# Performance work log

Measured on AMD Instinct MI355X. Metric: run time of the kernel, lower is better.

Reference implementation:

```python
import jax, jax.numpy as jnp
import numpy as np

N = 25000      # nodes
E = 400000     # edges (before self-loops)
D = 64         # input node feature dim
H = 4          # attention heads
C = 64         # out channels per head (concat=False -> head mean)
L = 3          # stacked layers
NEG_SLOPE = 0.2
EPS = 1e-5


def setup_inputs() -> dict:
    key = jax.random.key(0)
    ks = jax.random.split(key, 8)
    s = 0.1
    return {
        "x": jax.random.normal(ks[0], (N, D), jnp.float32),
        "edge_index": jax.random.randint(ks[1], (2, E), 0, N, dtype=jnp.int64),
        "Wl": jax.random.normal(ks[2], (L, H * C, D), jnp.float32) * s,
        "bl": jnp.zeros((L, H * C), jnp.float32),
        "Wr": jax.random.normal(ks[3], (L, H * C, D), jnp.float32) * s,
        "br": jnp.zeros((L, H * C), jnp.float32),
        "att": jax.random.normal(ks[4], (L, H, C), jnp.float32) * s,
        "conv_bias": jnp.zeros((L, C), jnp.float32),
        "gn_weight": jnp.ones((L, C), jnp.float32),
        "gn_scale": jnp.ones((L, C), jnp.float32),   # GraphNorm mean_scale (alpha)
        "gn_bias": jnp.zeros((L, C), jnp.float32),
    }


def _gat_forward(x, src, dst, Wl, bl, Wr, br, att, conv_bias,
                 gn_weight, gn_scale, gn_bias):
    n = x.shape[0]
    for i in range(L):
        # GATv2Conv (edge_attr=None, concat=False): separate source/target projections
        xl = (x @ Wl[i].T + bl[i]).reshape(n, H, C)  # [N,H,C]
        xr = (x @ Wr[i].T + br[i]).reshape(n, H, C)
        # per-edge attention logits: att . leaky_relu(xl[j] + xr[i])
        e = jax.nn.leaky_relu(xl[src] + xr[dst], NEG_SLOPE)      # [E',H,C]
        logits = jnp.einsum('ehc,hc->eh', e, att[i])             # [E',H]
        # segment softmax over incoming edges of each target node
        m = jax.ops.segment_max(logits, dst, num_segments=n)     # [N,H]
        a = jnp.exp(logits - m[dst])
        denom = jax.ops.segment_sum(a, dst, num_segments=n)      # [N,H]
        alpha = a / denom[dst]                                   # [E',H]
        # weighted scatter-add of source messages, mean over heads
        agg = jax.ops.segment_sum(xl[src] * alpha[:, :, None], dst,
                                  num_segments=n)                # [N,H,C]
        h = agg.mean(axis=1) + conv_bias[i]                      # [N,C]
        # GraphNorm (single graph): x - alpha*mean, scale by rstd
        mu = h.mean(axis=0)
        hc = h - gn_scale[i] * mu
        var = jnp.mean(hc * hc, axis=0)
        x = hc * jax.lax.rsqrt(var + EPS) * gn_weight[i] + gn_bias[i]
        # Dropout p=0 at eval -> identity
    return x


def reference(x, edge_index, Wl, bl, Wr, br, att, conv_bias,
              gn_weight, gn_scale, gn_bias):
    n = x.shape[0]
    loop = jnp.arange(n, dtype=edge_index.dtype)
    # PyG GATv2Conv adds self-loops by default
    src = jnp.concatenate([edge_index[0], loop])
    dst = jnp.concatenate([edge_index[1], loop])
    return _gat_forward(x, src, dst, Wl, bl, Wr, br, att, conv_bias,
                        gn_weight, gn_scale, gn_bias)
```

## Files before the change

### kernel.cpp

```cpp
#include <hip/hip_runtime.h>
#include <hip/hip_fp16.h>
#include <math.h>

#define HC   256
#define DD   64
#define CC   64
#define NLAY 3

#define RCAP    64
#define RCAP_SH 6

#define NBKT 64

typedef _Float16 h2 __attribute__((ext_vector_type(2)));
typedef _Float16 h4 __attribute__((ext_vector_type(4)));
typedef _Float16 h8 __attribute__((ext_vector_type(8)));
typedef float    f4 __attribute__((ext_vector_type(4)));
typedef float    f2 __attribute__((ext_vector_type(2)));

#define XSTR 72
#define OSTR 276

__global__ __launch_bounds__(256) void zero_kernel(int* __restrict__ counts,
                                                   float* __restrict__ spart,
                                                   int n) {
    int i = blockIdx.x * 256 + threadIdx.x;
    if (i < n) counts[i] = 0;
    if (i < NLAY * NBKT * 128) spart[i] = 0.f;
}

__global__ __launch_bounds__(256) void fill_kernel(const int* __restrict__ srcArr,
                                                   const int* __restrict__ dstArr,
                                                   int* __restrict__ counts,
                                                   int* __restrict__ csr_src,
                                                   int e, int n) {
    int i = blockIdx.x * 256 + threadIdx.x;
    if (i >= e + n) return;
    int s, d;
    if (i < e) { s = srcArr[i]; d = dstArr[i]; }
    else       { s = d = i - e; }
    int slot = atomicAdd(&counts[d], 1);
    if (slot < RCAP) csr_src[(d << RCAP_SH) + slot] = s;
}

__global__ __launch_bounds__(256) void proj_kernel(const float* __restrict__ x,
                                                   const float* __restrict__ Wl,
                                                   const float* __restrict__ bl,
                                                   const float* __restrict__ Wr,
                                                   const float* __restrict__ br,
                                                   __half* __restrict__ xl,
                                                   __half* __restrict__ xr, int n,
                                                   const float* __restrict__ spart,
                                                   const float* __restrict__ pgw,
                                                   const float* __restrict__ pgs,
                                                   const float* __restrict__ pgb) {
    __shared__ _Float16 xs[64 * XSTR];
    __shared__ _Float16 ws[256 * XSTR];
    __shared__ float nrm_a[64], nrm_b[64];
    __shared__ float sred[128];
    const int t  = threadIdx.x;
    const int n0 = blockIdx.x * 64;

    if (spart && t < 128) {
        float a = 0.f;
        #pragma unroll 8
        for (int r = 0; r < NBKT; ++r) a += spart[r * 128 + t];
        sred[t] = a;
    }
    __syncthreads();
    if (t < 64) {
        float a = 1.f, b = 0.f;
        if (spart) {
            float inv_n = 1.0f / (float)n;
            float mu  = sred[t] * inv_n;
            float eh2 = sred[64 + t] * inv_n;
            float al  = pgs[t];
            float var = eh2 - 2.f * al * mu * mu + al * al * mu * mu;
            float rstd = rsqrtf(var + 1e-5f);
            a = pgw[t] * rstd;
            b = pgb[t] - al * mu * a;
        }
        nrm_a[t] = a; nrm_b[t] = b;
    }
    __syncthreads();

    {
        const float* xb = x + (size_t)n0 * DD;
        const int limit = (n - n0) * DD;
        #pragma unroll
        for (int it = 0; it < 4; ++it) {
            int f = (it * 256 + t) * 4;
            float4 v = make_float4(0.f, 0.f, 0.f, 0.f);
            if (f + 3 < limit) v = *(const float4*)(xb + f);
            else {
                float tmp[4] = {0.f, 0.f, 0.f, 0.f};
                for (int q = 0; q < 4; ++q) if (f + q < limit) tmp[q] = xb[f + q];
                v = make_float4(tmp[0], tmp[1], tmp[2], tmp[3]);
            }
            int d = f & 63;
            const float4 a4 = *(const float4*)&nrm_a[d];
            const float4 b4 = *(const float4*)&nrm_b[d];
            h4 hv;
            hv.x = (_Float16)fmaf(v.x, a4.x, b4.x);
            hv.y = (_Float16)fmaf(v.y, a4.y, b4.y);
            hv.z = (_Float16)fmaf(v.z, a4.z, b4.z);
            hv.w = (_Float16)fmaf(v.w, a4.w, b4.w);
            *(h4*)&xs[(f >> 6) * XSTR + d] = hv;
        }
    }

    const int w = t >> 6, lane = t & 63, m = lane & 15, q = lane >> 4;

    h8 A0, A1;
    f4 acc[16];

    #define STAGE_W(Wsel)                                                     \
    {                                                                         \
        _Pragma("unroll")                                                     \
        for (int it = 0; it < 16; ++it) {                                     \
            int f = (it * 256 + t) * 4;                                       \
            float4 v = *(const float4*)((Wsel) + f);                          \
            h4 hv = { (_Float16)v.x, (_Float16)v.y, (_Float16)v.z,            \
                      (_Float16)v.w };                                        \
            *(h4*)&ws[(f >> 6) * XSTR + (f & 63)] = hv;                       \
        }                                                                     \
    }

    #define MFMA_PASS()                                                       \
    {                                                                         \
        _Pragma("unroll")                                                     \
        for (int ct = 0; ct < 16; ++ct) {                                     \
            const _Float16* brow = ws + (ct * 16 + m) * XSTR + q * 8;         \
            const h8 B0 = *(const h8*)brow;                                   \
            const h8 B1 = *(const h8*)(brow + 32);                            \
            f4 c = {0.f, 0.f, 0.f, 0.f};                                      \
            c = __builtin_amdgcn_mfma_f32_16x16x32_f16(A0, B0, c, 0, 0, 0);   \
            c = __builtin_amdgcn_mfma_f32_16x16x32_f16(A1, B1, c, 0, 0, 0);   \
            acc[ct] = c;                                                      \
        }                                                                     \
    }

    #define EPILOGUE(bsel, osel)                                              \
    {                                                                         \
        _Pragma("unroll")                                                     \
        for (int ct = 0; ct < 16; ++ct) {                                     \
            int ch = ct * 16 + m;                                             \
            float bv = (bsel)[ch];                                            \
            _Pragma("unroll")                                                 \
            for (int r = 0; r < 4; ++r)                                       \
                ws[(w * 16 + q * 4 + r) * OSTR + ch] =                        \
                    (_Float16)(acc[ct][r] + bv);                              \
        }                                                                     \
        __syncthreads();                                                      \
        _Pragma("unroll")                                                     \
        for (int it = 0; it < 8; ++it) {                                      \
            int f   = (it * 256 + t) * 8;                                     \
            int row = f >> 8, ch = f & 255;                                   \
            if (n0 + row < n)                                                 \
                *(uint4*)((osel) + (size_t)(n0 + row) * HC + ch) =            \
                    *(const uint4*)&ws[row * OSTR + ch];                      \
        }                                                                     \
    }

    STAGE_W(Wl)
    __syncthreads();
    {
        const _Float16* arow = xs + (w * 16 + m) * XSTR + q * 8;
        A0 = *(const h8*)arow;
        A1 = *(const h8*)(arow + 32);
    }
    MFMA_PASS()
    __syncthreads();
    EPILOGUE(bl, xl)
    __syncthreads();

    STAGE_W(Wr)
    __syncthreads();
    MFMA_PASS()
    __syncthreads();
    EPILOGUE(br, xr)

    #undef STAGE_W
    #undef MFMA_PASS
    #undef EPILOGUE
}

__global__ __launch_bounds__(256) void attn_kernel(const __half* __restrict__ xl,
                                                   const __half* __restrict__ xr,
                                                   const float* __restrict__ att,
                                                   const float* __restrict__ conv_bias,
                                                   const int* __restrict__ counts,
                                                   const int* __restrict__ csr_src,
                                                   float* __restrict__ h_out,
                                                   float* __restrict__ spart, int n) {
    __shared__ float ps[4][64], ps2[4][64];
    const int wave = threadIdx.x >> 6;
    const int l    = threadIdx.x & 63;
    const int v    = blockIdx.x * 4 + wave;
    const bool active = (v < n);

    const int e2 = l >> 5;
    const int h  = (l >> 3) & 3;
    const int co = l & 7;
    const int choff = h * CC + co * 8;

    if (active) {
        h2 xr2[4];
        *(uint4*)xr2 = *(const uint4*)(xr + (size_t)v * HC + choff);
        h2 at2[4];
        {
            const float* ap = att + choff;
            float4 a0 = *(const float4*)(ap);
            float4 a1 = *(const float4*)(ap + 4);
            at2[0] = (h2){(_Float16)a0.x, (_Float16)a0.y};
            at2[1] = (h2){(_Float16)a0.z, (_Float16)a0.w};
            at2[2] = (h2){(_Float16)a1.x, (_Float16)a1.y};
            at2[3] = (h2){(_Float16)a1.z, (_Float16)a1.w};
        }
        const _Float16 k02 = (_Float16)0.2f;

        const int rs = v << RCAP_SH;
        const int re = rs + counts[v];

        float s = 0.f;
        h2 acch[4];
        #pragma unroll
        for (int q = 0; q < 4; ++q) acch[q] = (h2){(_Float16)0.f, (_Float16)0.f};

        #define CLAMPI(i) (((i) < re) ? (i) : rs)

        uint4 r0 = *(const uint4*)(xl + (size_t)csr_src[CLAMPI(rs + e2)]     * HC + choff);
        uint4 r1 = *(const uint4*)(xl + (size_t)csr_src[CLAMPI(rs + 2 + e2)] * HC + choff);
        uint4 r2 = *(const uint4*)(xl + (size_t)csr_src[CLAMPI(rs + 4 + e2)] * HC + choff);
        int jnA = csr_src[CLAMPI(rs + 6 + e2)];
        int jnB = csr_src[CLAMPI(rs + 8 + e2)];
        int jnC = csr_src[CLAMPI(rs + 10 + e2)];

        #define STAGE(RBUF, JREG, VOFF, JOFF)                                 \
        {                                                                     \
            const uint4 cur = RBUF;                                           \
            RBUF = *(const uint4*)(xl + (size_t)JREG * HC + choff);           \
            JREG = csr_src[CLAMPI(k + JOFF + e2)];                            \
            const bool valid = (k + VOFF + e2) < re;                          \
            const h2* xh = (const h2*)&cur;                                   \
            h2 d2 = (h2){(_Float16)0.f, (_Float16)0.f};                      \
            _Pragma("unroll")                                                 \
            for (int q = 0; q < 4; ++q) {                                     \
                h2 tt = xh[q] + xr2[q];                                       \
                h2 lk = __builtin_elementwise_max(tt, tt * k02);              \
                d2 += lk * at2[q];                                            \
            }                                                                 \
            float p = (float)d2.x + (float)d2.y;                              \
            p += __shfl_xor(p, 1, 64);                                        \
            p += __shfl_xor(p, 2, 64);                                        \
            p += __shfl_xor(p, 4, 64);                                        \
            float pe = valid ? __expf(p) : 0.f;                               \
            s += pe;                                                          \
            const _Float16 peh = (_Float16)pe;                                \
            const h2 pe2 = (h2){peh, peh};                                    \
            _Pragma("unroll")                                                 \
            for (int q = 0; q < 4; ++q)                                       \
                acch[q] += pe2 * xh[q];                                       \
        }

        for (int k = rs; k < re; k += 6) {
            STAGE(r0, jnA, 0, 12)
            STAGE(r1, jnB, 2, 14)
            STAGE(r2, jnC, 4, 16)
        }
        #undef STAGE
        #undef CLAMPI

        s += __shfl_xor(s, 32, 64);
        const float inv = 1.f / s;
        float out8[8];
        #pragma unroll
        for (int q = 0; q < 8; ++q) {
            float av = (q & 1) ? (float)acch[q >> 1].y : (float)acch[q >> 1].x;
            float a = av + __shfl_xor(av, 32, 64);
            a *= inv;
            a += __shfl_xor(a, 8, 64);
            a += __shfl_xor(a, 16, 64);
            out8[q] = 0.25f * a;
        }
        if (l < 8) {
            const float4 cb0 = *(const float4*)(conv_bias + co * 8);
            const float4 cb1 = *(const float4*)(conv_bias + co * 8 + 4);
            float4 o0 = make_float4(out8[0] + cb0.x, out8[1] + cb0.y,
                                    out8[2] + cb0.z, out8[3] + cb0.w);
            float4 o1 = make_float4(out8[4] + cb1.x, out8[5] + cb1.y,
                                    out8[6] + cb1.z, out8[7] + cb1.w);
            float* op = h_out + (size_t)v * CC + co * 8;
            *(float4*)op       = o0;
            *(float4*)(op + 4) = o1;
            ps [wave][co * 8 + 0] = o0.x;  ps2[wave][co * 8 + 0] = o0.x * o0.x;
            ps [wave][co * 8 + 1] = o0.y;  ps2[wave][co * 8 + 1] = o0.y * o0.y;
            ps [wave][co * 8 + 2] = o0.z;  ps2[wave][co * 8 + 2] = o0.z * o0.z;
            ps [wave][co * 8 + 3] = o0.w;  ps2[wave][co * 8 + 3] = o0.w * o0.w;
            ps [wave][co * 8 + 4] = o1.x;  ps2[wave][co * 8 + 4] = o1.x * o1.x;
            ps [wave][co * 8 + 5] = o1.y;  ps2[wave][co * 8 + 5] = o1.y * o1.y;
            ps [wave][co * 8 + 6] = o1.z;  ps2[wave][co * 8 + 6] = o1.z * o1.z;
            ps [wave][co * 8 + 7] = o1.w;  ps2[wave][co * 8 + 7] = o1.w * o1.w;
        }
    } else if (l < 8) {
        #pragma unroll
        for (int q = 0; q < 8; ++q) { ps[wave][l * 8 + q] = 0.f; ps2[wave][l * 8 + q] = 0.f; }
    }
    __syncthreads();
    if (threadIdx.x < 128) {
        const int c = threadIdx.x & 63;
        const float (*src)[64] = (threadIdx.x < 64) ? ps : ps2;
        float sum = src[0][c] + src[1][c] + src[2][c] + src[3][c];
        atomicAdd(&spart[(blockIdx.x & (NBKT - 1)) * 128 +
                         ((threadIdx.x < 64) ? c : 64 + c)], sum);
    }
}

__global__ __launch_bounds__(256) void norm_kernel(const float* __restrict__ h,
                                                   const float* __restrict__ spart,
                                                   const float* __restrict__ gw,
                                                   const float* __restrict__ gs,
                                                   const float* __restrict__ gb,
                                                   float* __restrict__ out, int n) {
    __shared__ float sred[128];
    __shared__ float na[64], nb[64];
    int t = threadIdx.x;
    if (t < 128) {
        float a = 0.f;
        #pragma unroll 8
        for (int r = 0; r < NBKT; ++r) a += spart[r * 128 + t];
        sred[t] = a;
    }
    __syncthreads();
    if (t < 64) {
        float inv_n = 1.0f / (float)n;
        float mu  = sred[t] * inv_n;
        float eh2 = sred[64 + t] * inv_n;
        float a   = gs[t];
        float var = eh2 - 2.f * a * mu * mu + a * a * mu * mu;
        float rstd = rsqrtf(var + 1e-5f);
        na[t] = gw[t] * rstd;
        nb[t] = gb[t] - a * mu * gw[t] * rstd;
    }
    __syncthreads();
    int c = t & 63;
    float w = na[c], b = nb[c];
    int total = n * CC;
    for (int idx = blockIdx.x * 256 + t; idx < total; idx += gridDim.x * 256)
        out[idx] = fmaf(h[idx], w, b);
}

extern "C" void kernel_launch(void* const* d_in, const int* in_sizes, int n_in,
                              void* d_out, int out_size, void* d_ws, size_t ws_size,
                              hipStream_t stream) {
    const float* x0  = (const float*)d_in[0];
    const int*   ei  = (const int*)d_in[1];
    const float* Wl  = (const float*)d_in[2];
    const float* bl  = (const float*)d_in[3];
    const float* Wr  = (const float*)d_in[4];
    const float* br  = (const float*)d_in[5];
    const float* att = (const float*)d_in[6];
    const float* cb  = (const float*)d_in[7];
    const float* gw  = (const float*)d_in[8];
    const float* gs  = (const float*)d_in[9];
    const float* gb  = (const float*)d_in[10];

    const int n = in_sizes[0] / DD;
    const int e = in_sizes[1] / 2;
    const int* srcArr = ei;
    const int* dstArr = ei + e;

    char* w = (char*)d_ws;
    auto alloc = [&](size_t bytes) -> char* {
        char* p = w;
        w += (bytes + 255) & ~(size_t)255;
        return p;
    };
    __half* xl    = (__half*)alloc((size_t)n * HC * 2);
    __half* xr    = (__half*)alloc((size_t)n * HC * 2);
    float* hbuf   = (float*)alloc((size_t)n * CC * 4);
    int*   counts = (int*)  alloc((size_t)n * 4);
    int*   csr    = (int*)  alloc((size_t)n * RCAP * 4);
    float* spart  = (float*)alloc((size_t)NLAY * NBKT * 128 * 4);

    const int tot = e + n;
    hipLaunchKernelGGL(zero_kernel,  dim3((n + 255) / 256),   dim3(256), 0, stream,
                       counts, spart, n);
    hipLaunchKernelGGL(fill_kernel,  dim3((tot + 255) / 256), dim3(256), 0, stream,
                       srcArr, dstArr, counts, csr, e, n);

    for (int L = 0; L < NLAY; ++L) {
        const float* xin = (L == 0) ? x0 : hbuf;
        const int Lp = (L == 0) ? 0 : L - 1;
        const float* sp = (L == 0) ? nullptr : spart + (size_t)Lp * NBKT * 128;
        hipLaunchKernelGGL(proj_kernel, dim3((n + 63) / 64), dim3(256), 0, stream,
                           xin, Wl + (size_t)L * HC * DD, bl + L * HC,
                           Wr + (size_t)L * HC * DD, br + L * HC, xl, xr, n,
                           sp, gw + Lp * CC, gs + Lp * CC, gb + Lp * CC);
        hipLaunchKernelGGL(attn_kernel, dim3((n + 3) / 4), dim3(256), 0, stream,
                           xl, xr, att + L * HC, cb + L * CC, counts, csr, hbuf,
                           spart + (size_t)L * NBKT * 128, n);
    }
    hipLaunchKernelGGL(norm_kernel, dim3(512), dim3(256), 0, stream,
                       hbuf, spart + (size_t)(NLAY - 1) * NBKT * 128,
                       gw + (NLAY - 1) * CC, gs + (NLAY - 1) * CC,
                       gb + (NLAY - 1) * CC, (float*)d_out, n);
}
```

Baseline: 283.8 us.

## Split attention per head across blocks and add separate head-combine kernel

Each attention block now handles one head for four nodes, with each wave working through eight edges at a time instead of two edges across all four heads. Per-head results go to a half-precision buffer. A new combine kernel averages the heads, adds the bias and accumulates the GraphNorm statistics. This spreads the gather work over four times as many blocks and groups blocks by head to improve L2 locality on xl rows, at the cost of an extra kernel launch per layer and a round trip through the intermediate buffer. Low-degree nodes leave more lanes idle in each eight-edge group.

```diff
diff --git a/kernel.cpp b/kernel.cpp
--- a/kernel.cpp
+++ b/kernel.cpp
@@ -6,6 +6,7 @@
 #define DD   64
 #define CC   64
 #define NLAY 3
+#define NH   4
 
 #define RCAP    64
 #define RCAP_SH 6
@@ -188,131 +189,126 @@
 __global__ __launch_bounds__(256) void attn_kernel(const __half* __restrict__ xl,
                                                    const __half* __restrict__ xr,
                                                    const float* __restrict__ att,
-                                                   const float* __restrict__ conv_bias,
                                                    const int* __restrict__ counts,
                                                    const int* __restrict__ csr_src,
-                                                   float* __restrict__ h_out,
-                                                   float* __restrict__ spart, int n) {
-    __shared__ float ps[4][64], ps2[4][64];
+                                                   __half* __restrict__ ph, int n) {
+    const int wg   = blockIdx.x;
+    const int h    = (wg & 7) >> 1;
+    const int g    = (wg >> 3) * 2 + (wg & 1);
     const int wave = threadIdx.x >> 6;
     const int l    = threadIdx.x & 63;
-    const int v    = blockIdx.x * 4 + wave;
-    const bool active = (v < n);
-
-    const int e2 = l >> 5;
-    const int h  = (l >> 3) & 3;
+    const int v    = g * 4 + wave;
+    if (v >= n) return;
+
+    const int e8 = l >> 3;
     const int co = l & 7;
     const int choff = h * CC + co * 8;
 
-    if (active) {
-        h2 xr2[4];
-        *(uint4*)xr2 = *(const uint4*)(xr + (size_t)v * HC + choff);
-        h2 at2[4];
-        {
-            const float* ap = att + choff;
-            float4 a0 = *(const float4*)(ap);
-            float4 a1 = *(const float4*)(ap + 4);
-            at2[0] = (h2){(_Float16)a0.x, (_Float16)a0.y};
-            at2[1] = (h2){(_Float16)a0.z, (_Float16)a0.w};
-            at2[2] = (h2){(_Float16)a1.x, (_Float16)a1.y};
-            at2[3] = (h2){(_Float16)a1.z, (_Float16)a1.w};
-        }
-        const _Float16 k02 = (_Float16)0.2f;
-
-        const int rs = v << RCAP_SH;
-        const int re = rs + counts[v];
-
-        float s = 0.f;
-        h2 acch[4];
-        #pragma unroll
-        for (int q = 0; q < 4; ++q) acch[q] = (h2){(_Float16)0.f, (_Float16)0.f};
-
-        #define CLAMPI(i) (((i) < re) ? (i) : rs)
-
-        uint4 r0 = *(const uint4*)(xl + (size_t)csr_src[CLAMPI(rs + e2)]     * HC + choff);
-        uint4 r1 = *(const uint4*)(xl + (size_t)csr_src[CLAMPI(rs + 2 + e2)] * HC + choff);
-        uint4 r2 = *(const uint4*)(xl + (size_t)csr_src[CLAMPI(rs + 4 + e2)] * HC + choff);
-        int jnA = csr_src[CLAMPI(rs + 6 + e2)];
-        int jnB = csr_src[CLAMPI(rs + 8 + e2)];
-        int jnC = csr_src[CLAMPI(rs + 10 + e2)];
-
-        #define STAGE(RBUF, JREG, VOFF, JOFF)                                 \
-        {                                                                     \
-            const uint4 cur = RBUF;                                           \
-            RBUF = *(const uint4*)(xl + (size_t)JREG * HC + choff);           \
-            JREG = csr_src[CLAMPI(k + JOFF + e2)];                            \
-            const bool valid = (k + VOFF + e2) < re;                          \
-            const h2* xh = (const h2*)&cur;                                   \
-            h2 d2 = (h2){(_Float16)0.f, (_Float16)0.f};                      \
-            _Pragma("unroll")                                                 \
-            for (int q = 0; q < 4; ++q) {                                     \
-                h2 tt = xh[q] + xr2[q];                                       \
-                h2 lk = __builtin_elementwise_max(tt, tt * k02);              \
-                d2 += lk * at2[q];                                            \
-            }                                                                 \
-            float p = (float)d2.x + (float)d2.y;                              \
-            p += __shfl_xor(p, 1, 64);                                        \
-            p += __shfl_xor(p, 2, 64);                                        \
-            p += __shfl_xor(p, 4, 64);                                        \
-            float pe = valid ? __expf(p) : 0.f;                               \
-            s += pe;                                                          \
-            const _Float16 peh = (_Float16)pe;                                \
-            const h2 pe2 = (h2){peh, peh};                                    \
-            _Pragma("unroll")                                                 \
-            for (int q = 0; q < 4; ++q)                                       \
-                acch[q] += pe2 * xh[q];                                       \
-        }
-
-        for (int k = rs; k < re; k += 6) {
-            STAGE(r0, jnA, 0, 12)
-            STAGE(r1, jnB, 2, 14)
-            STAGE(r2, jnC, 4, 16)
-        }
-        #undef STAGE
-        #undef CLAMPI
-
-        s += __shfl_xor(s, 32, 64);
-        const float inv = 1.f / s;
-        float out8[8];
-        #pragma unroll
-        for (int q = 0; q < 8; ++q) {
-            float av = (q & 1) ? (float)acch[q >> 1].y : (float)acch[q >> 1].x;
-            float a = av + __shfl_xor(av, 32, 64);
-            a *= inv;
-            a += __shfl_xor(a, 8, 64);
-            a += __shfl_xor(a, 16, 64);
-            out8[q] = 0.25f * a;
-        }
-        if (l < 8) {
-            const float4 cb0 = *(const float4*)(conv_bias + co * 8);
-            const float4 cb1 = *(const float4*)(conv_bias + co * 8 + 4);
-            float4 o0 = make_float4(out8[0] + cb0.x, out8[1] + cb0.y,
-                                    out8[2] + cb0.z, out8[3] + cb0.w);
-            float4 o1 = make_float4(out8[4] + cb1.x, out8[5] + cb1.y,
-                                    out8[6] + cb1.z, out8[7] + cb1.w);
-            float* op = h_out + (size_t)v * CC + co * 8;
-            *(float4*)op       = o0;
-            *(float4*)(op + 4) = o1;
-            ps [wave][co * 8 + 0] = o0.x;  ps2[wave][co * 8 + 0] = o0.x * o0.x;
-            ps [wave][co * 8 + 1] = o0.y;  ps2[wave][co * 8 + 1] = o0.y * o0.y;
-            ps [wave][co * 8 + 2] = o0.z;  ps2[wave][co * 8 + 2] = o0.z * o0.z;
-            ps [wave][co * 8 + 3] = o0.w;  ps2[wave][co * 8 + 3] = o0.w * o0.w;
-            ps [wave][co * 8 + 4] = o1.x;  ps2[wave][co * 8 + 4] = o1.x * o1.x;
-            ps [wave][co * 8 + 5] = o1.y;  ps2[wave][co * 8 + 5] = o1.y * o1.y;
-            ps [wave][co * 8 + 6] = o1.z;  ps2[wave][co * 8 + 6] = o1.z * o1.z;
-            ps [wave][co * 8 + 7] = o1.w;  ps2[wave][co * 8 + 7] = o1.w * o1.w;
-        }
-    } else if (l < 8) {
-        #pragma unroll
-        for (int q = 0; q < 8; ++q) { ps[wave][l * 8 + q] = 0.f; ps2[wave][l * 8 + q] = 0.f; }
-    }
-    __syncthreads();
-    if (threadIdx.x < 128) {
-        const int c = threadIdx.x & 63;
-        const float (*src)[64] = (threadIdx.x < 64) ? ps : ps2;
-        float sum = src[0][c] + src[1][c] + src[2][c] + src[3][c];
-        atomicAdd(&spart[(blockIdx.x & (NBKT - 1)) * 128 +
-                         ((threadIdx.x < 64) ? c : 64 + c)], sum);
+    h2 xr2[4];
+    *(uint4*)xr2 = *(const uint4*)(xr + (size_t)v * HC + choff);
+    h2 at2[4];
+    {
+        const float* ap = att + choff;
+        float4 a0 = *(const float4*)(ap);
+        float4 a1 = *(const float4*)(ap + 4);
+        at2[0] = (h2){(_Float16)a0.x, (_Float16)a0.y};
+        at2[1] = (h2){(_Float16)a0.z, (_Float16)a0.w};
+        at2[2] = (h2){(_Float16)a1.x, (_Float16)a1.y};
+        at2[3] = (h2){(_Float16)a1.z, (_Float16)a1.w};
+    }
+    const _Float16 k02 = (_Float16)0.2f;
+
+    const int rs = v << RCAP_SH;
+    const int re = rs + counts[v];
+
+    float s = 0.f;
+    h2 acch[4];
+    #pragma unroll
+    for (int q = 0; q < 4; ++q) acch[q] = (h2){(_Float16)0.f, (_Float16)0.f};
+
+    #define CLAMPI(i) (((i) < re) ? (i) : rs)
+
+    uint4 r0 = *(const uint4*)(xl + (size_t)csr_src[CLAMPI(rs + e8)]     * HC + choff);
+    uint4 r1 = *(const uint4*)(xl + (size_t)csr_src[CLAMPI(rs + 8 + e8)] * HC + choff);
+    int jn = csr_src[CLAMPI(rs + 16 + e8)];
+
+    #define STAGE(RBUF, VOFF, JOFF)                                       \
+    {                                                                     \
+        const uint4 cur = RBUF;                                           \
+        RBUF = *(const uint4*)(xl + (size_t)jn * HC + choff);             \
+        jn = csr_src[CLAMPI(k + JOFF + e8)];                              \
+        const bool valid = (k + VOFF + e8) < re;                          \
+        const h2* xh = (const h2*)&cur;                                   \
+        h2 d2 = (h2){(_Float16)0.f, (_Float16)0.f};                      \
+        _Pragma("unroll")                                                 \
+        for (int q = 0; q < 4; ++q) {                                     \
+            h2 tt = xh[q] + xr2[q];                                       \
+            h2 lk = __builtin_elementwise_max(tt, tt * k02);              \
+            d2 += lk * at2[q];                                            \
+        }                                                                 \
+        float p = (float)d2.x + (float)d2.y;                              \
+        p += __shfl_xor(p, 1, 64);                                        \
+        p += __shfl_xor(p, 2, 64);                                        \
+        p += __shfl_xor(p, 4, 64);                                        \
+        float pe = valid ? __expf(p) : 0.f;                               \
+        s += pe;                                                          \
+        const _Float16 peh = (_Float16)pe;                                \
+        const h2 pe2 = (h2){peh, peh};                                    \
+        _Pragma("unroll")                                                 \
+        for (int q = 0; q < 4; ++q)                                       \
+            acch[q] += pe2 * xh[q];                                       \
+    }
+
+    for (int k = rs; k < re; k += 16) {
+        STAGE(r0, 0, 24)
+        STAGE(r1, 8, 32)
+    }
+    #undef STAGE
+    #undef CLAMPI
+
+    s += __shfl_xor(s, 8, 64);
+    s += __shfl_xor(s, 16, 64);
+    s += __shfl_xor(s, 32, 64);
+    const float inv = 1.f / s;
+    h8 hv;
+    #pragma unroll
+    for (int q = 0; q < 8; ++q) {
+        float av = (q & 1) ? (float)acch[q >> 1].y : (float)acch[q >> 1].x;
+        av += __shfl_xor(av, 8, 64);
+        av += __shfl_xor(av, 16, 64);
+        av += __shfl_xor(av, 32, 64);
+        hv[q] = (_Float16)(av * inv);
+    }
+    if (e8 == 0)
+        *(h8*)(ph + ((size_t)h * n + v) * CC + co * 8) = hv;
+}
+
+__global__ __launch_bounds__(256) void combine_kernel(const __half* __restrict__ ph,
+                                                      const float* __restrict__ cb,
+                                                      float* __restrict__ hbuf,
+                                                      float* __restrict__ spart,
+                                                      int n) {
+    int t = threadIdx.x;
+    int c = t & 63, r = t >> 6;
+    const float bias = cb[c];
+    float s = 0.f, s2 = 0.f;
+    for (int v = blockIdx.x * 4 + r; v < n; v += gridDim.x * 4) {
+        float a = 0.25f * ((float)ph[((size_t)0 * n + v) * CC + c] +
+                           (float)ph[((size_t)1 * n + v) * CC + c] +
+                           (float)ph[((size_t)2 * n + v) * CC + c] +
+                           (float)ph[((size_t)3 * n + v) * CC + c]) + bias;
+        hbuf[(size_t)v * CC + c] = a;
+        s += a; s2 += a * a;
+    }
+    __shared__ float l1[256], l2[256];
+    l1[t] = s; l2[t] = s2;
+    __syncthreads();
+    if (t < 64) {
+        s  = l1[t] + l1[64 + t] + l1[128 + t] + l1[192 + t];
+        s2 = l2[t] + l2[64 + t] + l2[128 + t] + l2[192 + t];
+        const int bkt = blockIdx.x & (NBKT - 1);
+        atomicAdd(&spart[bkt * 128 + c], s);
+        atomicAdd(&spart[bkt * 128 + 64 + c], s2);
     }
 }
 
@@ -378,12 +374,15 @@
     };
     __half* xl    = (__half*)alloc((size_t)n * HC * 2);
     __half* xr    = (__half*)alloc((size_t)n * HC * 2);
+    __half* ph    = (__half*)alloc((size_t)NH * n * CC * 2);
     float* hbuf   = (float*)alloc((size_t)n * CC * 4);
     int*   counts = (int*)  alloc((size_t)n * 4);
     int*   csr    = (int*)  alloc((size_t)n * RCAP * 4);
     float* spart  = (float*)alloc((size_t)NLAY * NBKT * 128 * 4);
 
     const int tot = e + n;
+    const int ngrp = (n + 3) / 4;
+    const int attn_blocks = ngrp * NH;
     hipLaunchKernelGGL(zero_kernel,  dim3((n + 255) / 256),   dim3(256), 0, stream,
                        counts, spart, n);
     hipLaunchKernelGGL(fill_kernel,  dim3((tot + 255) / 256), dim3(256), 0, stream,
@@ -397,8 +396,10 @@
                            xin, Wl + (size_t)L * HC * DD, bl + L * HC,
                            Wr + (size_t)L * HC * DD, br + L * HC, xl, xr, n,
                            sp, gw + Lp * CC, gs + Lp * CC, gb + Lp * CC);
-        hipLaunchKernelGGL(attn_kernel, dim3((n + 3) / 4), dim3(256), 0, stream,
-                           xl, xr, att + L * HC, cb + L * CC, counts, csr, hbuf,
+        hipLaunchKernelGGL(attn_kernel, dim3(attn_blocks), dim3(256), 0, stream,
+                           xl, xr, att + L * HC, counts, csr, ph, n);
+        hipLaunchKernelGGL(combine_kernel, dim3(128), dim3(256), 0, stream,
+                           ph, cb + L * CC, hbuf,
                            spart + (size_t)L * NBKT * 128, n);
     }
     hipLaunchKernelGGL(norm_kernel, dim3(512), dim3(256), 0, stream,
```

After: 365.7 us. 1.29x slower.
